# Optimization experiments

Hardware: AMD Instinct MI355X
Metric: run time of the kernel (lower is better)

Reference implementation:

```python
import jax, jax.numpy as jnp
import numpy as np
from jax import lax

N = 512      # num_nodes in the graph
FEAT = 128   # args.feat_dim (node tag vocab)
EMB = 64     # embedding_size (input_feat width = 2*EMB = 128, per node_order.repeat(1,128))
HID = 128    # args.hidden / LSTM hidden size
NMLP = 4


def setup_inputs() -> dict:
    key = jax.random.key(0)
    ks = jax.random.split(key, 12)
    s = 0.05
    return {
        "node_tags": jax.random.randint(ks[0], (N,), 0, FEAT),
        "adj": jax.random.uniform(ks[1], (N, N), dtype=jnp.float32),
        "label": jax.random.randint(ks[2], (1,), 0, 2),
        "W_emb": jax.random.normal(ks[3], (FEAT, EMB), jnp.float32) * s,
        "b_emb": jnp.zeros((EMB,), jnp.float32),
        "W_ih": jax.random.normal(ks[4], (4 * HID, 2 * EMB), jnp.float32) * s,
        "W_hh": jax.random.normal(ks[5], (4 * HID, HID), jnp.float32) * s,
        "b_ih": jnp.zeros((4 * HID,), jnp.float32),
        "b_hh": jnp.zeros((4 * HID,), jnp.float32),
        "W1s": jax.random.normal(ks[6], (NMLP, HID, HID), jnp.float32) * s,
        "b1s": jnp.zeros((NMLP, HID), jnp.float32),
        "W2s": jax.random.normal(ks[7], (NMLP, HID), jnp.float32) * s,
        "b2s": jnp.zeros((NMLP,), jnp.float32),
        "var_raw": jax.random.normal(ks[8], (NMLP,), jnp.float32) * s,
    }


def _node_orders(adj, key):
    """Greedy noisy random-walk ordering from every start node. [N,N] int32."""
    n = adj.shape[0]
    starts = jnp.arange(n)
    keys = jax.random.split(key, n)

    def one_start(start, k):
        mask0 = jnp.ones((n,), jnp.float32).at[start].set(0.0)

        def step(carry, t):
            cur, mask = carry
            noise = jax.random.uniform(jax.random.fold_in(k, t), (n,),
                                       minval=0.01, maxval=0.1)
            prob = jnp.exp(jnp.take(adj, cur, axis=0) + noise)
            prob = (prob / prob.sum()) * mask  # masked: visited -> 0
            nxt = jnp.argmax(prob)
            return (nxt, mask.at[nxt].set(0.0)), nxt

        _, rest = lax.scan(step, (start, mask0), jnp.arange(n - 1))
        return jnp.concatenate([start[None], rest])

    return jax.vmap(one_start)(starts, keys)


def _lstm(x, W_ih, W_hh, b_ih, b_hh):
    # x: [T, B, In] -> out [T, B, H]
    T, B, _ = x.shape
    H = W_hh.shape[1]
    b = b_ih + b_hh

    def step(carry, xt):
        h, c = carry
        gates = xt @ W_ih.T + h @ W_hh.T + b           # [B, 4H]
        i, f, g, o = jnp.split(gates, 4, axis=-1)      # torch gate order i,f,g,o
        c = jax.nn.sigmoid(f) * c + jax.nn.sigmoid(i) * jnp.tanh(g)
        h = jax.nn.sigmoid(o) * jnp.tanh(c)
        return (h, c), h

    h0 = jnp.zeros((B, H), x.dtype)
    _, out = lax.scan(step, (h0, h0), x)
    return out


def reference(node_tags, adj, label, W_emb, b_emb, W_ih, W_hh, b_ih, b_hh,
              W1s, b1s, W2s, b2s, var_raw):
    n = adj.shape[0]
    onehot = jax.nn.one_hot(node_tags, W_emb.shape[0], dtype=jnp.float32)
    node_feat = onehot @ W_emb + b_emb                       # [N, EMB]
    A = (adj > 0.5).astype(jnp.float32)                      # binary adjacency
    neigh_feat = (A @ onehot) @ W_emb + b_emb                # neighbor tag histogram -> embed
    input_feat = jnp.concatenate([node_feat, neigh_feat], 1) # [N, 2*EMB]

    orders = _node_orders(adj, jax.random.key(42))           # [Nstart, Nstep]
    batch = input_feat[orders]                               # [Nstart, Nstep, 2E]
    batch = jnp.transpose(batch, (1, 0, 2))                  # [T=N, B=N, 2E]

    out = _lstm(batch, W_ih, W_hh, b_ih, b_hh)               # [T, B, HID]
    embed = out.mean(axis=0)                                 # [N, HID]

    # 4-way ensemble MLP heads (batched over k)
    h = jax.nn.relu(jnp.einsum('nd,kdh->knh', embed, W1s) + b1s[:, None, :])
    logits = jnp.einsum('knh,kh->kn', h, W2s) + b2s[:, None] # [4, N]
    y = jax.nn.sigmoid(logits)
    lab = label[0].astype(jnp.float32)
    bce = -(lab * jax.nn.log_sigmoid(logits)
            + (1.0 - lab) * jax.nn.log_sigmoid(-logits)).mean(axis=1)  # [4]
    loss_ = bce.sum()

    var_w = jax.nn.softplus(var_raw)                         # per-head weight
    c = var_w / var_w.sum()
    y_ = (c[:, None] * y).sum(axis=0)                        # [N]
    return loss_, y_
```

## Files before the change

kernel.cpp:

```cpp
#include <hip/hip_runtime.h>
#include <hip/hip_bf16.h>
#include <stdint.h>

#define NN 512
#define FEAT 128
#define EMBD 64
#define HID 128

typedef float f32x4 __attribute__((ext_vector_type(4)));
typedef short s16x8 __attribute__((ext_vector_type(8)));

__device__ __forceinline__ uint32_t rotl32(uint32_t v, int s){ return (v << s) | (v >> (32 - s)); }

__device__ __forceinline__ void tf2x32(uint32_t k0, uint32_t k1, uint32_t x0, uint32_t x1,
                                       uint32_t &o0, uint32_t &o1){
  uint32_t k2 = k0 ^ k1 ^ 0x1BD11BDAu;
  x0 += k0; x1 += k1;
  x0+=x1; x1=rotl32(x1,13); x1^=x0;
  x0+=x1; x1=rotl32(x1,15); x1^=x0;
  x0+=x1; x1=rotl32(x1,26); x1^=x0;
  x0+=x1; x1=rotl32(x1, 6); x1^=x0;
  x0 += k1; x1 += k2 + 1u;
  x0+=x1; x1=rotl32(x1,17); x1^=x0;
  x0+=x1; x1=rotl32(x1,29); x1^=x0;
  x0+=x1; x1=rotl32(x1,16); x1^=x0;
  x0+=x1; x1=rotl32(x1,24); x1^=x0;
  x0 += k2; x1 += k0 + 2u;
  x0+=x1; x1=rotl32(x1,13); x1^=x0;
  x0+=x1; x1=rotl32(x1,15); x1^=x0;
  x0+=x1; x1=rotl32(x1,26); x1^=x0;
  x0+=x1; x1=rotl32(x1, 6); x1^=x0;
  x0 += k0; x1 += k1 + 3u;
  x0+=x1; x1=rotl32(x1,17); x1^=x0;
  x0+=x1; x1=rotl32(x1,29); x1^=x0;
  x0+=x1; x1=rotl32(x1,16); x1^=x0;
  x0+=x1; x1=rotl32(x1,24); x1^=x0;
  x0 += k1; x1 += k2 + 4u;
  x0+=x1; x1=rotl32(x1,13); x1^=x0;
  x0+=x1; x1=rotl32(x1,15); x1^=x0;
  x0+=x1; x1=rotl32(x1,26); x1^=x0;
  x0+=x1; x1=rotl32(x1, 6); x1^=x0;
  x0 += k2; x1 += k0 + 5u;
  o0 = x0; o1 = x1;
}

__device__ __forceinline__ float bits_to_noise(uint32_t bits){
  float u = __builtin_bit_cast(float, (bits >> 9) | 0x3f800000u) - 1.0f;
  const float dlt = 0.1f - 0.01f;
  float v = __fadd_rn(__fmul_rn(u, dlt), 0.01f);
  return fmaxf(0.01f, v);
}

__device__ __forceinline__ short f2bf(float f){
  uint32_t u = __builtin_bit_cast(uint32_t, f);
  u += 0x7fffu + ((u >> 16) & 1u);
  return (short)(u >> 16);
}

__device__ __forceinline__ float fsig(float x){
  return __builtin_amdgcn_rcpf(1.0f + __expf(-x));
}
__device__ __forceinline__ float ftanh(float x){
  float e = __expf(2.0f * x);
  return 1.0f - 2.0f * __builtin_amdgcn_rcpf(e + 1.0f);
}
__device__ __forceinline__ float softplusf(float x){
  return log1pf(expf(x));
}

__device__ __forceinline__ void lds_barrier(){
  asm volatile("s_waitcnt lgkmcnt(0)\n\ts_barrier" ::: "memory");
}

__device__ __forceinline__ float wave_fmax(float x){
  int xi;
  #define DSTEP(C) xi = __builtin_amdgcn_update_dpp(0, __builtin_bit_cast(int,x), C, 0xF, 0xF, true); \
                   x = fmaxf(x, __builtin_bit_cast(float,xi));
  DSTEP(0xB1)
  DSTEP(0x4E)
  DSTEP(0x141)
  DSTEP(0x140)
  #undef DSTEP
  xi = __builtin_amdgcn_ds_swizzle(__builtin_bit_cast(int,x), 0x401F);
  x = fmaxf(x, __builtin_bit_cast(float,xi));
  x = fmaxf(x, __shfl_xor(x, 32));
  return x;
}
__device__ __forceinline__ uint32_t wave_maxu(uint32_t x){
  int m;
  #define USTEP(C) m = __builtin_amdgcn_update_dpp(0, (int)x, C, 0xF, 0xF, true); \
                   x = x > (uint32_t)m ? x : (uint32_t)m;
  USTEP(0xB1) USTEP(0x4E) USTEP(0x141) USTEP(0x140)
  #undef USTEP
  m = __builtin_amdgcn_ds_swizzle((int)x, 0x401F);
  x = x > (uint32_t)m ? x : (uint32_t)m;
  uint32_t o = (uint32_t)__shfl_xor((int)x, 32);
  x = x > o ? x : o;
  return x;
}

__device__ __forceinline__ void orders_body(const float* __restrict__ adj,
                                            int* __restrict__ orders, int s){
  int lane = threadIdx.x;
  __shared__ uint32_t kts[2*(NN-1)];
  __shared__ uint32_t pcs[NN];

  uint32_t ks0, ks1; tf2x32(0u, 42u, 0u, (uint32_t)s, ks0, ks1);
  for (int t = lane; t < NN-1; t += 64){
    uint32_t a, b; tf2x32(ks0, ks1, 0u, (uint32_t)t, a, b);
    kts[2*t] = a; kts[2*t+1] = b;
  }
  __syncthreads();

  uint32_t vis = 0;
  if ((s >> 3) == lane) vis |= 1u << (s & 7);
  if (lane == 0) orders[(size_t)s*NN] = s;
  unsigned long long lt = (1ull << lane) - 1ull;

  const float4* r4 = (const float4*)(adj + (size_t)s*NN);
  float4 v0 = r4[lane*2], v1 = r4[lane*2+1];

  for (int t = 0; t < NN-1; ++t){
    uint32_t kt0 = kts[2*t], kt1 = kts[2*t+1];
    float a[8] = {v0.x,v0.y,v0.z,v0.w,v1.x,v1.y,v1.z,v1.w};

    float mx = -1.f;
    #pragma unroll
    for (int e = 0; e < 8; ++e)
      mx = fmaxf(mx, ((vis >> e) & 1) ? -1.f : a[e]);
    mx = wave_fmax(mx);
    float T = mx - 0.0901f;

    int base = 0, pos[8]; uint32_t cm = 0;
    #pragma unroll
    for (int e = 0; e < 8; ++e){
      bool c = !((vis >> e) & 1) && (a[e] >= T);
      unsigned long long bal = __ballot(c);
      pos[e] = base + __popcll(bal & lt);
      base += __popcll(bal);
      if (c) cm |= 1u << e;
    }
    #pragma unroll
    for (int e = 0; e < 8; ++e)
      if ((cm >> e) & 1){
        uint32_t a23 = (uint32_t)(a[e] * 8388608.0f);
        pcs[pos[e]] = (a23 << 9) | (uint32_t)(lane*8 + e);
      }
    int total = base;

    uint32_t bk = 0; int bi = 0x7fffffff;
    for (int b0 = 0; b0 < total; b0 += 64){
      int k = b0 + lane;
      if (k < total){
        uint32_t pc = pcs[k];
        int idx = (int)(pc & 511u);
        uint32_t x0, x1;
        tf2x32(kt0, kt1, 0u, (uint32_t)idx, x0, x1);
        float nz = bits_to_noise(x0 ^ x1);
        uint32_t n30 = (uint32_t)(nz * 1073741824.0f);
        uint32_t key = ((pc >> 9) << 7) + n30;
        if (key > bk || (key == bk && idx < bi)){ bk = key; bi = idx; }
      }
    }
    uint32_t km = wave_maxu(bk);
    unsigned long long msk = __ballot(bk == km);
    int widx;
    if (__popcll(msk) == 1){
      widx = __shfl(bi, __ffsll((long long)msk) - 1);
    } else {
      int iv = (bk == km) ? bi : 0x7fffffff;
      #pragma unroll
      for (int off = 1; off < 64; off <<= 1){
        int o = __shfl_xor(iv, off);
        iv = o < iv ? o : iv;
      }
      widx = iv;
    }
    const float4* nr = (const float4*)(adj + (size_t)widx*NN);
    v0 = nr[lane*2]; v1 = nr[lane*2+1];
    if ((widx >> 3) == lane) vis |= 1u << (widx & 7);
    if (lane == 0) orders[(size_t)s*NN + t + 1] = widx;
  }
}

__device__ __forceinline__ void featifw_body(int n, const int* __restrict__ tags,
    const float* __restrict__ adj, const float* __restrict__ W_emb,
    const float* __restrict__ b_emb, const float* __restrict__ W_ih,
    const float* __restrict__ b_ih, const float* __restrict__ b_hh,
    float* __restrict__ IFW){
  int tid = threadIdx.x;
  __shared__ int tg[NN];
  __shared__ __align__(16) float xs[2*EMBD];
  for (int i = tid; i < NN; i += 64) tg[i] = tags[i];
  float nf = W_emb[tg[n]*EMBD + tid] + b_emb[tid];
  float ac = 0.f;
  for (int m = 0; m < NN; ++m){
    if (adj[(size_t)n*NN + m] > 0.5f) ac += W_emb[tg[m]*EMBD + tid];
  }
  xs[tid]        = nf;
  xs[EMBD + tid] = ac + b_emb[tid];
  __syncthreads();
  const float4* xs4 = (const float4*)xs;
  for (int it = 0; it < 8; ++it){
    int g = it*64 + tid;
    const float4* wr4 = (const float4*)(W_ih + (size_t)g*(2*EMBD));
    float a2 = b_ih[g] + b_hh[g];
    #pragma unroll 8
    for (int kk = 0; kk < 32; ++kk){
      float4 wv = wr4[kk], xv = xs4[kk];
      a2 += wv.x*xv.x + wv.y*xv.y + wv.z*xv.z + wv.w*xv.w;
    }
    IFW[(size_t)n*(4*HID) + (g & 127)*4 + (g >> 7)] = a2;
  }
}

__global__ __launch_bounds__(64) void k_mega1(const float* __restrict__ adj,
    int* __restrict__ orders, const int* __restrict__ tags,
    const float* __restrict__ W_emb, const float* __restrict__ b_emb,
    const float* __restrict__ W_ih, const float* __restrict__ b_ih,
    const float* __restrict__ b_hh, float* __restrict__ IFW){
  if (blockIdx.x < NN) orders_body(adj, orders, blockIdx.x);
  else                 featifw_body(blockIdx.x - NN, tags, adj, W_emb, b_emb,
                                    W_ih, b_ih, b_hh, IFW);
}

__global__ __launch_bounds__(512, 2) void k_lstm(const float* __restrict__ W_hh,
    const float* __restrict__ IFW2, const int* __restrict__ orders,
    const float* __restrict__ W1s, const float* __restrict__ b1s,
    const float* __restrict__ W2s, const float* __restrict__ b2s,
    float* __restrict__ logits){
  int wg = blockIdx.x, tid = threadIdx.x;
  int w = tid >> 6, l = tid & 63, l15 = l & 15, l4 = l >> 4;
  int em = tid >> 7, eu = tid & 127;

  __shared__ int ord_s[4*NN];
  __shared__ __align__(16) short hbuf[16][HID+8];
  __shared__ __align__(16) float gl[4][520];
  __shared__ float part[4][2];

  for (int i = tid; i < 4*NN; i += 512)
    ord_s[i] = orders[(size_t)(4*wg)*NN + i];
  for (int i = tid; i < 16*(HID+8); i += 512)
    ((short*)hbuf)[i] = 0;

  s16x8 Bf[4][4];
  #pragma unroll
  for (int q = 0; q < 4; ++q)
    #pragma unroll
    for (int kt = 0; kt < 4; ++kt){
      int g = q*HID + w*16 + l15;
      const float* src = W_hh + (size_t)g*HID + kt*32 + l4*8;
      s16x8 v;
      #pragma unroll
      for (int e = 0; e < 8; ++e) v[e] = f2bf(src[e]);
      Bf[q][kt] = v;
    }
  __syncthreads();

  int u = w*16 + l15;
  float cst = 0.f, emb = 0.f;

  f32x4 vif[4];
  if (l4 == 0){
    #pragma unroll
    for (int r = 0; r < 4; ++r)
      vif[r] = *(const f32x4*)(IFW2 + (size_t)ord_s[r*NN]*(4*HID) + u*4);
  }

  for (int t = 0; t < NN; ++t){
    s16x8 Af[4];
    #pragma unroll
    for (int kt = 0; kt < 4; ++kt)
      Af[kt] = *(const s16x8*)&hbuf[l15][kt*32 + l4*8];

    f32x4 acc[4];
    #pragma unroll
    for (int q = 0; q < 4; ++q){
      f32x4 a = {0.f, 0.f, 0.f, 0.f};
      #pragma unroll
      for (int kt = 0; kt < 4; ++kt)
        a = __builtin_amdgcn_mfma_f32_16x16x32_bf16(Af[kt], Bf[q][kt], a, 0, 0, 0);
      acc[q] = a;
    }

    int tn = (t + 1 < NN) ? t + 1 : NN - 1;
    f32x4 vifn[4];
    if (l4 == 0){
      #pragma unroll
      for (int r = 0; r < 4; ++r)
        vifn[r] = *(const f32x4*)(IFW2 + (size_t)ord_s[r*NN + tn]*(4*HID) + u*4);
      #pragma unroll
      for (int q = 0; q < 4; ++q)
        #pragma unroll
        for (int r = 0; r < 4; ++r)
          gl[r][u*4 + q] = acc[q][r] + vif[r][q];
    }
    lds_barrier();

    f32x4 g4 = *(const f32x4*)&gl[em][eu*4];
    float si = fsig(g4[0]);
    float sf = fsig(g4[1]);
    float tg = ftanh(g4[2]);
    float so = fsig(g4[3]);
    float cn = sf * cst + si * tg;
    cst = cn;
    float h = so * ftanh(cn);
    emb += h;
    hbuf[em][eu] = f2bf(h);
    #pragma unroll
    for (int r = 0; r < 4; ++r) vif[r] = vifn[r];
    lds_barrier();
  }

  float* eL = (float*)gl;
  eL[em*HID + eu] = emb * (1.0f/512.0f);
  __syncthreads();

  int hk = tid >> 7;
  int uu = tid & 127;
  float b1v = b1s[hk*HID + uu];
  float w2v = W2s[hk*HID + uu];
  const float* wcol = W1s + (size_t)hk*HID*HID + uu;
  for (int m = 0; m < 4; ++m){
    const float4* es4 = (const float4*)(eL + m*HID);
    float pre = b1v;
    #pragma unroll 4
    for (int d4 = 0; d4 < 32; ++d4){
      float4 e4 = es4[d4];
      pre += e4.x * wcol[(4*d4+0)*HID];
      pre += e4.y * wcol[(4*d4+1)*HID];
      pre += e4.z * wcol[(4*d4+2)*HID];
      pre += e4.w * wcol[(4*d4+3)*HID];
    }
    float v = fmaxf(pre, 0.f) * w2v;
    #pragma unroll
    for (int off = 1; off < 64; off <<= 1) v += __shfl_xor(v, off);
    if (l == 0) part[hk][(tid >> 6) & 1] = v;
    __syncthreads();
    if (tid < 4) logits[tid*NN + 4*wg + m] = part[tid][0] + part[tid][1] + b2s[tid];
    __syncthreads();
  }
}

__global__ __launch_bounds__(512) void k_final(const float* __restrict__ logits,
                                               const int* __restrict__ label,
                                               const float* __restrict__ var_raw,
                                               float* __restrict__ out){
  int n = threadIdx.x;
  float lab = (float)label[0];
  float sp[4]; float tot = 0.f;
  #pragma unroll
  for (int k = 0; k < 4; ++k){ sp[k] = softplusf(var_raw[k]); tot += sp[k]; }
  float y = 0.f, bce = 0.f;
  #pragma unroll
  for (int k = 0; k < 4; ++k){
    float x = logits[k*NN + n];
    float yk = 1.0f / (1.0f + expf(-x));
    y += (sp[k] / tot) * yk;
    bce += lab * softplusf(-x) + (1.0f - lab) * softplusf(x);
  }
  out[1 + n] = y;
  __shared__ float pr[8];
  #pragma unroll
  for (int off = 1; off < 64; off <<= 1) bce += __shfl_xor(bce, off);
  if ((n & 63) == 0) pr[n >> 6] = bce;
  __syncthreads();
  if (n == 0){
    float ssum = 0.f;
    for (int i = 0; i < 8; ++i) ssum += pr[i];
    out[0] = ssum * (1.0f/512.0f);
  }
}

extern "C" void kernel_launch(void* const* d_in, const int* in_sizes, int n_in,
                              void* d_out, int out_size, void* d_ws, size_t ws_size,
                              hipStream_t stream) {
  const int*   node_tags = (const int*)  d_in[0];
  const float* adj       = (const float*)d_in[1];
  const int*   label     = (const int*)  d_in[2];
  const float* W_emb     = (const float*)d_in[3];
  const float* b_emb     = (const float*)d_in[4];
  const float* W_ih      = (const float*)d_in[5];
  const float* W_hh      = (const float*)d_in[6];
  const float* b_ih      = (const float*)d_in[7];
  const float* b_hh      = (const float*)d_in[8];
  const float* W1s       = (const float*)d_in[9];
  const float* b1s       = (const float*)d_in[10];
  const float* W2s       = (const float*)d_in[11];
  const float* b2s       = (const float*)d_in[12];
  const float* var_raw   = (const float*)d_in[13];
  float* out = (float*)d_out;

  float* ws     = (float*)d_ws;
  float* IFW    = ws + 65536;
  float* logits = IFW + 262144 + 65536;
  int*   orders = (int*)(logits + 2048);

  k_mega1<<<dim3(2*NN), dim3(64), 0, stream>>>(adj, orders, node_tags, W_emb,
                                               b_emb, W_ih, b_ih, b_hh, IFW);
  k_lstm <<<dim3(128), dim3(512), 0, stream>>>(W_hh, IFW, orders, W1s, b1s,
                                               W2s, b2s, logits);
  k_final<<<dim3(1),   dim3(512), 0, stream>>>(logits, label, var_raw, out);
}
```

Measured before the change: 1.103 ms.

## Batch 16 LSTM sequences per MFMA and pack 16 walks per block

The LSTM kernel now handles 16 batch columns per workgroup instead of 4. It swaps the MFMA operands so each lane owns 4 hidden units across the batch and applies the gate nonlinearities straight from the accumulators. This removes the LDS gate scatter and one barrier per step, and a double-buffered h tile leaves one barrier per step. The ordering/feature kernel packs 16 independent waves into 1024-thread blocks and computes the per-step Threefry keys on the fly rather than precomputing them into LDS. The trade-off is far fewer blocks (32 LSTM workgroups, 64 preprocessing blocks) and less parallelism across CUs.

After: 1.954 ms. 77.2% more time.

```diff
diff --git a/kernel.cpp b/kernel.cpp
--- a/kernel.cpp
+++ b/kernel.cpp
@@ -8,6 +8,7 @@
 #define HID 128
 
 typedef float f32x4 __attribute__((ext_vector_type(4)));
+typedef short s16x4 __attribute__((ext_vector_type(4)));
 typedef short s16x8 __attribute__((ext_vector_type(8)));
 
 __device__ __forceinline__ uint32_t rotl32(uint32_t v, int s){ return (v << s) | (v >> (32 - s)); }
@@ -99,151 +100,143 @@
   return x;
 }
 
-__device__ __forceinline__ void orders_body(const float* __restrict__ adj,
-                                            int* __restrict__ orders, int s){
-  int lane = threadIdx.x;
-  __shared__ uint32_t kts[2*(NN-1)];
-  __shared__ uint32_t pcs[NN];
-
-  uint32_t ks0, ks1; tf2x32(0u, 42u, 0u, (uint32_t)s, ks0, ks1);
-  for (int t = lane; t < NN-1; t += 64){
-    uint32_t a, b; tf2x32(ks0, ks1, 0u, (uint32_t)t, a, b);
-    kts[2*t] = a; kts[2*t+1] = b;
-  }
-  __syncthreads();
-
-  uint32_t vis = 0;
-  if ((s >> 3) == lane) vis |= 1u << (s & 7);
-  if (lane == 0) orders[(size_t)s*NN] = s;
-  unsigned long long lt = (1ull << lane) - 1ull;
-
-  const float4* r4 = (const float4*)(adj + (size_t)s*NN);
-  float4 v0 = r4[lane*2], v1 = r4[lane*2+1];
-
-  for (int t = 0; t < NN-1; ++t){
-    uint32_t kt0 = kts[2*t], kt1 = kts[2*t+1];
-    float a[8] = {v0.x,v0.y,v0.z,v0.w,v1.x,v1.y,v1.z,v1.w};
-
-    float mx = -1.f;
-    #pragma unroll
-    for (int e = 0; e < 8; ++e)
-      mx = fmaxf(mx, ((vis >> e) & 1) ? -1.f : a[e]);
-    mx = wave_fmax(mx);
-    float T = mx - 0.0901f;
-
-    int base = 0, pos[8]; uint32_t cm = 0;
-    #pragma unroll
-    for (int e = 0; e < 8; ++e){
-      bool c = !((vis >> e) & 1) && (a[e] >= T);
-      unsigned long long bal = __ballot(c);
-      pos[e] = base + __popcll(bal & lt);
-      base += __popcll(bal);
-      if (c) cm |= 1u << e;
-    }
-    #pragma unroll
-    for (int e = 0; e < 8; ++e)
-      if ((cm >> e) & 1){
-        uint32_t a23 = (uint32_t)(a[e] * 8388608.0f);
-        pcs[pos[e]] = (a23 << 9) | (uint32_t)(lane*8 + e);
-      }
-    int total = base;
-
-    uint32_t bk = 0; int bi = 0x7fffffff;
-    for (int b0 = 0; b0 < total; b0 += 64){
-      int k = b0 + lane;
-      if (k < total){
-        uint32_t pc = pcs[k];
-        int idx = (int)(pc & 511u);
-        uint32_t x0, x1;
-        tf2x32(kt0, kt1, 0u, (uint32_t)idx, x0, x1);
-        float nz = bits_to_noise(x0 ^ x1);
-        uint32_t n30 = (uint32_t)(nz * 1073741824.0f);
-        uint32_t key = ((pc >> 9) << 7) + n30;
-        if (key > bk || (key == bk && idx < bi)){ bk = key; bi = idx; }
-      }
-    }
-    uint32_t km = wave_maxu(bk);
-    unsigned long long msk = __ballot(bk == km);
-    int widx;
-    if (__popcll(msk) == 1){
-      widx = __shfl(bi, __ffsll((long long)msk) - 1);
-    } else {
-      int iv = (bk == km) ? bi : 0x7fffffff;
-      #pragma unroll
-      for (int off = 1; off < 64; off <<= 1){
-        int o = __shfl_xor(iv, off);
-        iv = o < iv ? o : iv;
-      }
-      widx = iv;
-    }
-    const float4* nr = (const float4*)(adj + (size_t)widx*NN);
-    v0 = nr[lane*2]; v1 = nr[lane*2+1];
-    if ((widx >> 3) == lane) vis |= 1u << (widx & 7);
-    if (lane == 0) orders[(size_t)s*NN + t + 1] = widx;
-  }
-}
-
-__device__ __forceinline__ void featifw_body(int n, const int* __restrict__ tags,
-    const float* __restrict__ adj, const float* __restrict__ W_emb,
-    const float* __restrict__ b_emb, const float* __restrict__ W_ih,
-    const float* __restrict__ b_ih, const float* __restrict__ b_hh,
-    float* __restrict__ IFW){
-  int tid = threadIdx.x;
-  __shared__ int tg[NN];
-  __shared__ __align__(16) float xs[2*EMBD];
-  for (int i = tid; i < NN; i += 64) tg[i] = tags[i];
-  float nf = W_emb[tg[n]*EMBD + tid] + b_emb[tid];
-  float ac = 0.f;
-  for (int m = 0; m < NN; ++m){
-    if (adj[(size_t)n*NN + m] > 0.5f) ac += W_emb[tg[m]*EMBD + tid];
-  }
-  xs[tid]        = nf;
-  xs[EMBD + tid] = ac + b_emb[tid];
-  __syncthreads();
-  const float4* xs4 = (const float4*)xs;
-  for (int it = 0; it < 8; ++it){
-    int g = it*64 + tid;
-    const float4* wr4 = (const float4*)(W_ih + (size_t)g*(2*EMBD));
-    float a2 = b_ih[g] + b_hh[g];
-    #pragma unroll 8
-    for (int kk = 0; kk < 32; ++kk){
-      float4 wv = wr4[kk], xv = xs4[kk];
-      a2 += wv.x*xv.x + wv.y*xv.y + wv.z*xv.z + wv.w*xv.w;
-    }
-    IFW[(size_t)n*(4*HID) + (g & 127)*4 + (g >> 7)] = a2;
-  }
-}
-
-__global__ __launch_bounds__(64) void k_mega1(const float* __restrict__ adj,
+__global__ __launch_bounds__(1024) void k_mega1(const float* __restrict__ adj,
     int* __restrict__ orders, const int* __restrict__ tags,
     const float* __restrict__ W_emb, const float* __restrict__ b_emb,
     const float* __restrict__ W_ih, const float* __restrict__ b_ih,
     const float* __restrict__ b_hh, float* __restrict__ IFW){
-  if (blockIdx.x < NN) orders_body(adj, orders, blockIdx.x);
-  else                 featifw_body(blockIdx.x - NN, tags, adj, W_emb, b_emb,
-                                    W_ih, b_ih, b_hh, IFW);
-}
-
-__global__ __launch_bounds__(512, 2) void k_lstm(const float* __restrict__ W_hh,
+  int bid = blockIdx.x, tid = threadIdx.x;
+  int wave = tid >> 6, lane = tid & 63;
+
+  __shared__ uint32_t pcs_all[16][NN];
+  __shared__ int tg[NN];
+  __shared__ __align__(16) float xs_all[16][2*EMBD];
+
+  if (bid < 32){
+    int s = bid*16 + wave;
+    uint32_t* pcs = pcs_all[wave];
+    int s_u = __builtin_amdgcn_readfirstlane(s);
+    uint32_t ks0, ks1; tf2x32(0u, 42u, 0u, (uint32_t)s_u, ks0, ks1);
+    uint32_t ktc0, ktc1; tf2x32(ks0, ks1, 0u, 0u, ktc0, ktc1);
+
+    uint32_t vis = 0;
+    if ((s >> 3) == lane) vis |= 1u << (s & 7);
+    if (lane == 0) orders[(size_t)s*NN] = s;
+    unsigned long long lt = (1ull << lane) - 1ull;
+
+    const float4* r4 = (const float4*)(adj + (size_t)s*NN);
+    float4 v0 = r4[lane*2], v1 = r4[lane*2+1];
+
+    for (int t = 0; t < NN-1; ++t){
+      uint32_t kt0 = ktc0, kt1 = ktc1;
+      tf2x32(ks0, ks1, 0u, (uint32_t)(t+1), ktc0, ktc1);
+
+      float a[8] = {v0.x,v0.y,v0.z,v0.w,v1.x,v1.y,v1.z,v1.w};
+      float mx = -1.f;
+      #pragma unroll
+      for (int e = 0; e < 8; ++e)
+        mx = fmaxf(mx, ((vis >> e) & 1) ? -1.f : a[e]);
+      mx = wave_fmax(mx);
+      float T = mx - 0.0901f;
+
+      int base = 0, pos[8]; uint32_t cm = 0;
+      #pragma unroll
+      for (int e = 0; e < 8; ++e){
+        bool c = !((vis >> e) & 1) && (a[e] >= T);
+        unsigned long long bal = __ballot(c);
+        pos[e] = base + __popcll(bal & lt);
+        base += __popcll(bal);
+        if (c) cm |= 1u << e;
+      }
+      #pragma unroll
+      for (int e = 0; e < 8; ++e)
+        if ((cm >> e) & 1){
+          uint32_t a23 = (uint32_t)(a[e] * 8388608.0f);
+          pcs[pos[e]] = (a23 << 9) | (uint32_t)(lane*8 + e);
+        }
+      int total = base;
+
+      uint32_t bk = 0; int bi = 0x7fffffff;
+      for (int b0 = 0; b0 < total; b0 += 64){
+        int k = b0 + lane;
+        if (k < total){
+          uint32_t pc = pcs[k];
+          int idx = (int)(pc & 511u);
+          uint32_t x0, x1;
+          tf2x32(kt0, kt1, 0u, (uint32_t)idx, x0, x1);
+          float nz = bits_to_noise(x0 ^ x1);
+          uint32_t n30 = (uint32_t)(nz * 1073741824.0f);
+          uint32_t key = ((pc >> 9) << 7) + n30;
+          if (key > bk || (key == bk && idx < bi)){ bk = key; bi = idx; }
+        }
+      }
+      uint32_t km = wave_maxu(bk);
+      unsigned long long msk = __ballot(bk == km);
+      int widx;
+      if (__popcll(msk) == 1){
+        widx = __shfl(bi, __ffsll((long long)msk) - 1);
+      } else {
+        int iv = (bk == km) ? bi : 0x7fffffff;
+        #pragma unroll
+        for (int off = 1; off < 64; off <<= 1){
+          int o = __shfl_xor(iv, off);
+          iv = o < iv ? o : iv;
+        }
+        widx = iv;
+      }
+      const float4* nr = (const float4*)(adj + (size_t)widx*NN);
+      v0 = nr[lane*2]; v1 = nr[lane*2+1];
+      if ((widx >> 3) == lane) vis |= 1u << (widx & 7);
+      if (lane == 0) orders[(size_t)s*NN + t + 1] = widx;
+    }
+  } else {
+    for (int i = tid; i < NN; i += 1024) tg[i] = tags[i];
+    __syncthreads();
+    int n = (bid - 32)*16 + wave;
+    float* xs = xs_all[wave];
+    float nf = W_emb[tg[n]*EMBD + lane] + b_emb[lane];
+    float ac = 0.f;
+    const float* row = adj + (size_t)n*NN;
+    for (int m = 0; m < NN; ++m){
+      if (row[m] > 0.5f) ac += W_emb[tg[m]*EMBD + lane];
+    }
+    xs[lane]        = nf;
+    xs[EMBD + lane] = ac + b_emb[lane];
+    const float4* xs4 = (const float4*)xs;
+    for (int it = 0; it < 8; ++it){
+      int g = it*64 + lane;
+      const float4* wr4 = (const float4*)(W_ih + (size_t)g*(2*EMBD));
+      float a2 = b_ih[g] + b_hh[g];
+      #pragma unroll 8
+      for (int kk = 0; kk < 32; ++kk){
+        float4 wv = wr4[kk], xv = xs4[kk];
+        a2 += wv.x*xv.x + wv.y*xv.y + wv.z*xv.z + wv.w*xv.w;
+      }
+      IFW[(size_t)n*(4*HID) + (g & 127)*4 + (g >> 7)] = a2;
+    }
+  }
+}
+
+__global__ __launch_bounds__(512, 1) void k_lstm(const float* __restrict__ W_hh,
     const float* __restrict__ IFW2, const int* __restrict__ orders,
     const float* __restrict__ W1s, const float* __restrict__ b1s,
     const float* __restrict__ W2s, const float* __restrict__ b2s,
     float* __restrict__ logits){
   int wg = blockIdx.x, tid = threadIdx.x;
   int w = tid >> 6, l = tid & 63, l15 = l & 15, l4 = l >> 4;
-  int em = tid >> 7, eu = tid & 127;
-
-  __shared__ int ord_s[4*NN];
-  __shared__ __align__(16) short hbuf[16][HID+8];
-  __shared__ __align__(16) float gl[4][520];
+
+  __shared__ int ord_s[NN*16];
+  __shared__ __align__(16) short hbuf[2][16][HID+8];
   __shared__ float part[4][2];
 
-  for (int i = tid; i < 4*NN; i += 512)
-    ord_s[i] = orders[(size_t)(4*wg)*NN + i];
-  for (int i = tid; i < 16*(HID+8); i += 512)
+  for (int i = tid; i < NN*16; i += 512){
+    int t = i >> 4, m = i & 15;
+    ord_s[i] = orders[(size_t)(16*wg + m)*NN + t];
+  }
+  for (int i = tid; i < 2*16*(HID+8); i += 512)
     ((short*)hbuf)[i] = 0;
 
-  s16x8 Bf[4][4];
+  s16x8 Wf[4][4];
   #pragma unroll
   for (int q = 0; q < 4; ++q)
     #pragma unroll
@@ -253,25 +246,36 @@
       s16x8 v;
       #pragma unroll
       for (int e = 0; e < 8; ++e) v[e] = f2bf(src[e]);
-      Bf[q][kt] = v;
+      Wf[q][kt] = v;
     }
   __syncthreads();
 
-  int u = w*16 + l15;
-  float cst = 0.f, emb = 0.f;
-
-  f32x4 vif[4];
-  if (l4 == 0){
-    #pragma unroll
-    for (int r = 0; r < 4; ++r)
-      vif[r] = *(const f32x4*)(IFW2 + (size_t)ord_s[r*NN]*(4*HID) + u*4);
+  int ubase = w*16 + l4*4;
+  float c[4] = {0,0,0,0}, emb[4] = {0,0,0,0};
+
+  f32x4 vif[4], vifn[4];
+  {
+    int ord = ord_s[l15];
+    const float* base = IFW2 + (size_t)ord*(4*HID) + ubase*4;
+    #pragma unroll
+    for (int r = 0; r < 4; ++r) vif[r] = *(const f32x4*)(base + r*4);
   }
 
   for (int t = 0; t < NN; ++t){
-    s16x8 Af[4];
+    int pb = t & 1, wb = 1 - pb;
+
+    int tn = (t + 1 < NN) ? t + 1 : NN - 1;
+    {
+      int ord = ord_s[tn*16 + l15];
+      const float* base = IFW2 + (size_t)ord*(4*HID) + ubase*4;
+      #pragma unroll
+      for (int r = 0; r < 4; ++r) vifn[r] = *(const f32x4*)(base + r*4);
+    }
+
+    s16x8 Hf[4];
     #pragma unroll
     for (int kt = 0; kt < 4; ++kt)
-      Af[kt] = *(const s16x8*)&hbuf[l15][kt*32 + l4*8];
+      Hf[kt] = *(const s16x8*)&hbuf[pb][l15][kt*32 + l4*8];
 
     f32x4 acc[4];
     #pragma unroll
@@ -279,41 +283,38 @@
       f32x4 a = {0.f, 0.f, 0.f, 0.f};
       #pragma unroll
       for (int kt = 0; kt < 4; ++kt)
-        a = __builtin_amdgcn_mfma_f32_16x16x32_bf16(Af[kt], Bf[q][kt], a, 0, 0, 0);
+        a = __builtin_amdgcn_mfma_f32_16x16x32_bf16(Wf[q][kt], Hf[kt], a, 0, 0, 0);
       acc[q] = a;
     }
 
-    int tn = (t + 1 < NN) ? t + 1 : NN - 1;
-    f32x4 vifn[4];
-    if (l4 == 0){
-      #pragma unroll
-      for (int r = 0; r < 4; ++r)
-        vifn[r] = *(const f32x4*)(IFW2 + (size_t)ord_s[r*NN + tn]*(4*HID) + u*4);
-      #pragma unroll
-      for (int q = 0; q < 4; ++q)
-        #pragma unroll
-        for (int r = 0; r < 4; ++r)
-          gl[r][u*4 + q] = acc[q][r] + vif[r][q];
-    }
-    lds_barrier();
-
-    f32x4 g4 = *(const f32x4*)&gl[em][eu*4];
-    float si = fsig(g4[0]);
-    float sf = fsig(g4[1]);
-    float tg = ftanh(g4[2]);
-    float so = fsig(g4[3]);
-    float cn = sf * cst + si * tg;
-    cst = cn;
-    float h = so * ftanh(cn);
-    emb += h;
-    hbuf[em][eu] = f2bf(h);
+    s16x4 hp;
+    #pragma unroll
+    for (int r = 0; r < 4; ++r){
+      float gi = acc[0][r] + vif[r][0];
+      float gf = acc[1][r] + vif[r][1];
+      float gg = acc[2][r] + vif[r][2];
+      float go = acc[3][r] + vif[r][3];
+      float si = fsig(gi), sf = fsig(gf), so = fsig(go);
+      float tg = ftanh(gg);
+      float cn = sf * c[r] + si * tg;
+      c[r] = cn;
+      float h = so * ftanh(cn);
+      emb[r] += h;
+      hp[r] = f2bf(h);
+    }
+    *(s16x4*)&hbuf[wb][l15][ubase] = hp;
     #pragma unroll
     for (int r = 0; r < 4; ++r) vif[r] = vifn[r];
     lds_barrier();
   }
 
-  float* eL = (float*)gl;
-  eL[em*HID + eu] = emb * (1.0f/512.0f);
+  float* eL = (float*)ord_s;
+  __syncthreads();
+  {
+    f32x4 ev = {emb[0]*(1.0f/512.0f), emb[1]*(1.0f/512.0f),
+                emb[2]*(1.0f/512.0f), emb[3]*(1.0f/512.0f)};
+    *(f32x4*)&eL[l15*HID + ubase] = ev;
+  }
   __syncthreads();
 
   int hk = tid >> 7;
@@ -321,7 +322,7 @@
   float b1v = b1s[hk*HID + uu];
   float w2v = W2s[hk*HID + uu];
   const float* wcol = W1s + (size_t)hk*HID*HID + uu;
-  for (int m = 0; m < 4; ++m){
+  for (int m = 0; m < 16; ++m){
     const float4* es4 = (const float4*)(eL + m*HID);
     float pre = b1v;
     #pragma unroll 4
@@ -337,7 +338,7 @@
     for (int off = 1; off < 64; off <<= 1) v += __shfl_xor(v, off);
     if (l == 0) part[hk][(tid >> 6) & 1] = v;
     __syncthreads();
-    if (tid < 4) logits[tid*NN + 4*wg + m] = part[tid][0] + part[tid][1] + b2s[tid];
+    if (tid < 4) logits[tid*NN + 16*wg + m] = part[tid][0] + part[tid][1] + b2s[tid];
     __syncthreads();
   }
 }
@@ -396,9 +397,9 @@
   float* logits = IFW + 262144 + 65536;
   int*   orders = (int*)(logits + 2048);
 
-  k_mega1<<<dim3(2*NN), dim3(64), 0, stream>>>(adj, orders, node_tags, W_emb,
-                                               b_emb, W_ih, b_ih, b_hh, IFW);
-  k_lstm <<<dim3(128), dim3(512), 0, stream>>>(W_hh, IFW, orders, W1s, b1s,
-                                               W2s, b2s, logits);
-  k_final<<<dim3(1),   dim3(512), 0, stream>>>(logits, label, var_raw, out);
-}
+  k_mega1<<<dim3(64),  dim3(1024), 0, stream>>>(adj, orders, node_tags, W_emb,
+                                                b_emb, W_ih, b_ih, b_hh, IFW);
+  k_lstm <<<dim3(32),  dim3(512),  0, stream>>>(W_hh, IFW, orders, W1s, b1s,
+                                                W2s, b2s, logits);
+  k_final<<<dim3(1),   dim3(512),  0, stream>>>(logits, label, var_raw, out);
+}
```
